# Kernel tuning notes

Hardware: AMD Instinct MI355X
Metric: run time of the kernel (lower is better)

## Reference

```python
import jax, jax.numpy as jnp
import numpy as np

N = 4096          # in_features
M = 4096          # out_features
RANK = 64
FT = 16           # ft_rank (trainable LoRA)
RES = RANK - FT   # frozen low-rank residual
CB = 65536        # E8P: 16-bit codeword per group of 8 weights
CW = 8            # codeword width (E8 lattice dim)
Q_SCALE = 0.02
GLOBAL_SCALE = 1.0


def _hadamard(n):
    # Sylvester construction, normalized: H @ H.T = I (matches matmul_hadU/hadUt up to transpose; H is symmetric)
    H = np.array([[1.0]], dtype=np.float32)
    while H.shape[0] < n:
        H = np.block([[H, H], [H, -H]])
    return H / np.sqrt(np.float32(n))


def setup_inputs() -> dict:
    key = jax.random.key(0)
    ks = jax.random.split(key, 9)
    x = jax.random.normal(ks[0], (8192, N), jnp.float32)
    Q_idxs = jax.random.randint(ks[1], (M, N // CW), 0, CB, dtype=jnp.int32)
    grid = jax.random.normal(ks[2], (CB, CW), jnp.float32) * 0.5   # E8P codebook grid
    SU = jax.random.rademacher(ks[3], (N,), dtype=jnp.float32)     # random sign vectors (QuIP#)
    SV = jax.random.rademacher(ks[4], (M,), dtype=jnp.float32)
    L_ft = jax.random.normal(ks[5], (M, FT), jnp.float32) * 0.02
    R_ft = jax.random.normal(ks[6], (FT, N), jnp.float32) * 0.02
    L_res = jax.random.normal(ks[7], (M, RES), jnp.float32) * 0.02
    R_res = jax.random.normal(ks[8], (RES, N), jnp.float32) * 0.02
    had_left = jnp.asarray(_hadamard(N))
    had_right = jnp.asarray(_hadamard(M))
    return {"x": x, "SU": SU, "SV": SV, "grid": grid, "L_ft": L_ft, "R_ft": R_ft,
            "L_res": L_res, "R_res": R_res, "had_left": had_left,
            "had_right": had_right, "Q_idxs": Q_idxs}


def reference(x, SU, SV, grid, L_ft, R_ft, L_res, R_res, had_left, had_right, Q_idxs):
    shape = x.shape
    h = x.reshape(-1, N) * SU                 # x * SU
    h = h @ had_left                          # matmul_hadUt (Hadamard is symmetric orthogonal)
    # E8P codebook decode: gather 8-dim codewords -> full [M, N] weight, fused matmul
    W = grid[Q_idxs].reshape(M, N)            # [M, N//8, 8] -> [M, N]
    out = (h @ W.T) * Q_SCALE                 # Q.forward
    out = out + (h @ R_res.T) @ L_res.T       # frozen low-rank residual (rank - ft_rank)
    out = out + (h @ R_ft.T) @ L_ft.T         # trainable LoRA path
    out = (out @ had_right) * GLOBAL_SCALE    # matmul_hadU * global_scale
    out = out * SV
    return out.reshape(*shape[:-1], M)
```

## Files before the change

kernel.cpp:

```cpp
#include <hip/hip_runtime.h>
#include <hip/hip_bf16.h>
#include <stdint.h>


typedef __bf16 bf16;
typedef __bf16 bf16x8 __attribute__((ext_vector_type(8)));
typedef float f32x4 __attribute__((ext_vector_type(4)));

#define KE 4160
#define KT_MAIN 130
#define NN 4096
#define MM 4096
#define BB 8192

__global__ void prep_kernel(const float* __restrict__ Lft, const float* __restrict__ Rft,
                            const float* __restrict__ Lres, const float* __restrict__ Rres,
                            bf16* __restrict__ Rcat, bf16* __restrict__ Wq) {
  int tid = blockIdx.x * 256 + threadIdx.x;
  if (tid < 64 * 4096) {
    int r = tid >> 12, n = tid & 4095;
    float v = (r < 48) ? Rres[r * 4096 + n] : Rft[(r - 48) * 4096 + n];
    Rcat[tid] = (bf16)v;
  } else {
    int t2 = tid - 64 * 4096;
    int m = t2 >> 6, r = t2 & 63;
    float v = (r < 48) ? Lres[m * 48 + r] : Lft[m * 16 + (r - 48)];
    Wq[(size_t)m * KE + 4096 + r] = (bf16)v;
  }
}

__global__ void decode_kernel(const int* __restrict__ qidx, const float* __restrict__ grid,
                              bf16* __restrict__ Wq) {
  int tid = blockIdx.x * 256 + threadIdx.x;
  int m = tid >> 9, g = tid & 511;
  uint32_t idx = (uint32_t)qidx[tid];
  const float4* gp = (const float4*)(grid + (size_t)idx * 8);
  float4 w0 = gp[0], w1 = gp[1];
  bf16x8 o;
  o[0] = (bf16)(w0.x * 0.02f); o[1] = (bf16)(w0.y * 0.02f);
  o[2] = (bf16)(w0.z * 0.02f); o[3] = (bf16)(w0.w * 0.02f);
  o[4] = (bf16)(w1.x * 0.02f); o[5] = (bf16)(w1.y * 0.02f);
  o[6] = (bf16)(w1.z * 0.02f); o[7] = (bf16)(w1.w * 0.02f);
  *(bf16x8*)(Wq + (size_t)m * KE + g * 8) = o;
}

__global__ void fwht_pre_kernel(const float* __restrict__ src,
                                bf16* __restrict__ dst,
                                const float* __restrict__ SU) {
  __shared__ float buf[4096];
  const int row = blockIdx.x, t = threadIdx.x;
  const float4* sp = (const float4*)(src + (size_t)row * NN + t * 16);
  const float4* su = (const float4*)(SU + t * 16);
  float v[16];
#pragma unroll
  for (int q = 0; q < 4; ++q) {
    float4 a = sp[q], s = su[q];
    v[q * 4 + 0] = a.x * s.x; v[q * 4 + 1] = a.y * s.y;
    v[q * 4 + 2] = a.z * s.z; v[q * 4 + 3] = a.w * s.w;
  }
#pragma unroll
  for (int s = 1; s < 16; s <<= 1) {
#pragma unroll
    for (int i = 0; i < 16; ++i) {
      if (!(i & s)) { float a = v[i], b = v[i + s]; v[i] = a + b; v[i + s] = a - b; }
    }
  }
#pragma unroll
  for (int i = 0; i < 16; ++i) buf[t * 16 + i] = v[i];
  for (int s = 16; s < 4096; s <<= 1) {
    __syncthreads();
#pragma unroll
    for (int j = 0; j < 8; ++j) {
      int p = t + j * 256;
      int i = ((p & ~(s - 1)) << 1) | (p & (s - 1));
      float a = buf[i], b = buf[i + s];
      buf[i] = a + b; buf[i + s] = a - b;
    }
  }
  __syncthreads();
  bf16x8 o0, o1;
#pragma unroll
  for (int i = 0; i < 8; ++i) {
    o0[i] = (bf16)(buf[t * 16 + i] * 0.015625f);
    o1[i] = (bf16)(buf[t * 16 + 8 + i] * 0.015625f);
  }
  bf16* dp = dst + (size_t)row * KE + t * 16;
  *(bf16x8*)dp = o0;
  *(bf16x8*)(dp + 8) = o1;
}

__global__ void fwht_post_kernel(float* __restrict__ data, const float* __restrict__ SV) {
  __shared__ float buf[4096];
  const int row = blockIdx.x, t = threadIdx.x;
  float4* dp = (float4*)(data + (size_t)row * MM + t * 16);
  float v[16];
#pragma unroll
  for (int q = 0; q < 4; ++q) {
    float4 a = dp[q];
    v[q * 4 + 0] = a.x; v[q * 4 + 1] = a.y; v[q * 4 + 2] = a.z; v[q * 4 + 3] = a.w;
  }
#pragma unroll
  for (int s = 1; s < 16; s <<= 1) {
#pragma unroll
    for (int i = 0; i < 16; ++i) {
      if (!(i & s)) { float a = v[i], b = v[i + s]; v[i] = a + b; v[i + s] = a - b; }
    }
  }
#pragma unroll
  for (int i = 0; i < 16; ++i) buf[t * 16 + i] = v[i];
  for (int s = 16; s < 4096; s <<= 1) {
    __syncthreads();
#pragma unroll
    for (int j = 0; j < 8; ++j) {
      int p = t + j * 256;
      int i = ((p & ~(s - 1)) << 1) | (p & (s - 1));
      float a = buf[i], b = buf[i + s];
      buf[i] = a + b; buf[i + s] = a - b;
    }
  }
  __syncthreads();
  const float4* sv = (const float4*)(SV + t * 16);
#pragma unroll
  for (int q = 0; q < 4; ++q) {
    float4 s = sv[q];
    float4 o;
    o.x = buf[t * 16 + q * 4 + 0] * 0.015625f * s.x;
    o.y = buf[t * 16 + q * 4 + 1] * 0.015625f * s.y;
    o.z = buf[t * 16 + q * 4 + 2] * 0.015625f * s.z;
    o.w = buf[t * 16 + q * 4 + 3] * 0.015625f * s.w;
    dp[q] = o;
  }
}

__global__ void __launch_bounds__(256) tgemm_kernel(const bf16* __restrict__ A,
                                                    const bf16* __restrict__ Bm,
                                                    float* __restrict__ Tpart) {
  __shared__ bf16 lA[128 * 32];
  __shared__ bf16 lB[64 * 32];
  const int t = threadIdx.x, w = t >> 6, l = t & 63;
  const int bmBlk = blockIdx.x;
  const int split = blockIdx.y;
  const int wm = w >> 1, wn = w & 1;
  f32x4 acc[4][2] = {};
  const int arow = t >> 1, acol = (t & 1) * 16;
  const bf16* pa = A + (size_t)(bmBlk * 128 + arow) * KE + acol;
  const int brow = (t & 127) >> 1, bcol = acol;
  const bf16* pb = Bm + (size_t)brow * 4096 + bcol;
  const int fr = l & 15, fk = (l >> 4) * 8;
  for (int kt = 0; kt < 32; ++kt) {
    const int k0 = (split * 32 + kt) * 32;
    bf16x8 a0 = *(const bf16x8*)(pa + k0);
    bf16x8 a1 = *(const bf16x8*)(pa + k0 + 8);
    *(bf16x8*)&lA[arow * 32 + acol] = a0;
    *(bf16x8*)&lA[arow * 32 + acol + 8] = a1;
    if (t < 128) {
      bf16x8 b0 = *(const bf16x8*)(pb + k0);
      bf16x8 b1 = *(const bf16x8*)(pb + k0 + 8);
      *(bf16x8*)&lB[brow * 32 + bcol] = b0;
      *(bf16x8*)&lB[brow * 32 + bcol + 8] = b1;
    }
    __syncthreads();
    bf16x8 af[4], bfr[2];
#pragma unroll
    for (int i = 0; i < 4; ++i) af[i] = *(const bf16x8*)&lA[(wm * 64 + i * 16 + fr) * 32 + fk];
#pragma unroll
    for (int i = 0; i < 2; ++i) bfr[i] = *(const bf16x8*)&lB[(wn * 32 + i * 16 + fr) * 32 + fk];
#pragma unroll
    for (int mi = 0; mi < 4; ++mi)
#pragma unroll
      for (int ni = 0; ni < 2; ++ni)
        acc[mi][ni] = __builtin_amdgcn_mfma_f32_16x16x32_bf16(af[mi], bfr[ni], acc[mi][ni], 0, 0, 0);
    __syncthreads();
  }
  float* out = Tpart + (size_t)split * BB * 64;
  const int orow = bmBlk * 128 + wm * 64 + (l >> 4) * 4;
  const int ocol = wn * 32 + (l & 15);
#pragma unroll
  for (int mi = 0; mi < 4; ++mi)
#pragma unroll
    for (int ni = 0; ni < 2; ++ni)
#pragma unroll
      for (int r = 0; r < 4; ++r)
        out[(size_t)(orow + mi * 16 + r) * 64 + ocol + ni * 16] = acc[mi][ni][r];
}

__global__ void tconv_kernel(const float* __restrict__ Tpart, bf16* __restrict__ h) {
  int i = blockIdx.x * 256 + threadIdx.x;
  float s = Tpart[i] + Tpart[i + BB * 64] + Tpart[i + 2 * BB * 64] + Tpart[i + 3 * BB * 64];
  int row = i >> 6, c = i & 63;
  h[(size_t)row * KE + 4096 + c] = (bf16)s;
}

__global__ void __launch_bounds__(256) mgemm_kernel(const bf16* __restrict__ A,
                                                    const bf16* __restrict__ B,
                                                    float* __restrict__ C) {
  __shared__ bf16 lA[128 * 32];
  __shared__ bf16 lB[128 * 32];
  const int t = threadIdx.x, w = t >> 6, l = t & 63;
  const int bn = blockIdx.x, bm = blockIdx.y;
  const int wm = w >> 1, wn = w & 1;
  f32x4 acc[4][4] = {};
  const int srow = t >> 1, scol = (t & 1) * 16;
  const bf16* pa = A + (size_t)(bm * 128 + srow) * KE + scol;
  const bf16* pb = B + (size_t)(bn * 128 + srow) * KE + scol;
  const int fr = l & 15, fk = (l >> 4) * 8;
  for (int kt = 0; kt < KT_MAIN; ++kt) {
    const int k0 = kt * 32;
    bf16x8 a0 = *(const bf16x8*)(pa + k0);
    bf16x8 a1 = *(const bf16x8*)(pa + k0 + 8);
    bf16x8 b0 = *(const bf16x8*)(pb + k0);
    bf16x8 b1 = *(const bf16x8*)(pb + k0 + 8);
    *(bf16x8*)&lA[srow * 32 + scol] = a0;
    *(bf16x8*)&lA[srow * 32 + scol + 8] = a1;
    *(bf16x8*)&lB[srow * 32 + scol] = b0;
    *(bf16x8*)&lB[srow * 32 + scol + 8] = b1;
    __syncthreads();
    bf16x8 af[4], bfr[4];
#pragma unroll
    for (int i = 0; i < 4; ++i) {
      af[i] = *(const bf16x8*)&lA[(wm * 64 + i * 16 + fr) * 32 + fk];
      bfr[i] = *(const bf16x8*)&lB[(wn * 64 + i * 16 + fr) * 32 + fk];
    }
#pragma unroll
    for (int mi = 0; mi < 4; ++mi)
#pragma unroll
      for (int ni = 0; ni < 4; ++ni)
        acc[mi][ni] = __builtin_amdgcn_mfma_f32_16x16x32_bf16(af[mi], bfr[ni], acc[mi][ni], 0, 0, 0);
    __syncthreads();
  }
  const int orow = bm * 128 + wm * 64 + (l >> 4) * 4;
  const int ocol = bn * 128 + wn * 64 + (l & 15);
#pragma unroll
  for (int mi = 0; mi < 4; ++mi)
#pragma unroll
    for (int ni = 0; ni < 4; ++ni)
#pragma unroll
      for (int r = 0; r < 4; ++r)
        C[(size_t)(orow + mi * 16 + r) * MM + ocol + ni * 16] = acc[mi][ni][r];
}

extern "C" void kernel_launch(void* const* d_in, const int* in_sizes, int n_in,
                              void* d_out, int out_size, void* d_ws, size_t ws_size,
                              hipStream_t stream) {
  const float* x    = (const float*)d_in[0];
  const float* SU   = (const float*)d_in[1];
  const float* SV   = (const float*)d_in[2];
  const float* grid = (const float*)d_in[3];
  const float* Lft  = (const float*)d_in[4];
  const float* Rft  = (const float*)d_in[5];
  const float* Lres = (const float*)d_in[6];
  const float* Rres = (const float*)d_in[7];
  const int*   qidx = (const int*)d_in[10];
  float* out = (float*)d_out;

  char* ws = (char*)d_ws;
  bf16*  h     = (bf16*)ws;
  bf16*  Wq    = (bf16*)(ws + 68157440);
  bf16*  Rcat  = (bf16*)(ws + 68157440 + 34078720);
  float* Tpart = (float*)(ws + 68157440 + 34078720 + 524288);

  prep_kernel<<<2048, 256, 0, stream>>>(Lft, Rft, Lres, Rres, Rcat, Wq);
  decode_kernel<<<8192, 256, 0, stream>>>(qidx, grid, Wq);
  fwht_pre_kernel<<<8192, 256, 0, stream>>>(x, h, SU);
  tgemm_kernel<<<dim3(64, 4), 256, 0, stream>>>(h, Rcat, Tpart);
  tconv_kernel<<<2048, 256, 0, stream>>>(Tpart, h);
  mgemm_kernel<<<dim3(32, 64), 256, 0, stream>>>(h, Wq, out);
  fwht_post_kernel<<<8192, 256, 0, stream>>>(out, SV);
}
```

Before: 753.2 us.

## Double-buffer LDS tiles in main GEMM with register prefetch of next k-tile

The main bf16 GEMM now keeps two LDS buffers per operand. The next k-tile is loaded from global memory into registers before the current tile's MFMAs run, and stored into the alternate buffer afterwards, with a single barrier per iteration. This is meant to hide global-load latency behind compute and remove one of the two barriers per k-step. It doubles shared memory use and adds some register pressure, which could reduce occupancy.

After: 760.1 us. Within noise of the previous version (+0.9%).

```diff
diff --git a/kernel.cpp b/kernel.cpp
--- a/kernel.cpp
+++ b/kernel.cpp
@@ -194,8 +194,8 @@
 __global__ void __launch_bounds__(256) mgemm_kernel(const bf16* __restrict__ A,
                                                     const bf16* __restrict__ B,
                                                     float* __restrict__ C) {
-  __shared__ bf16 lA[128 * 32];
-  __shared__ bf16 lB[128 * 32];
+  __shared__ bf16 lA[2][128 * 32];
+  __shared__ bf16 lB[2][128 * 32];
   const int t = threadIdx.x, w = t >> 6, l = t & 63;
   const int bn = blockIdx.x, bm = blockIdx.y;
   const int wm = w >> 1, wn = w & 1;
@@ -204,29 +204,46 @@
   const bf16* pa = A + (size_t)(bm * 128 + srow) * KE + scol;
   const bf16* pb = B + (size_t)(bn * 128 + srow) * KE + scol;
   const int fr = l & 15, fk = (l >> 4) * 8;
+  const int so = srow * 32 + scol;
+
+  bf16x8 a0 = *(const bf16x8*)(pa);
+  bf16x8 a1 = *(const bf16x8*)(pa + 8);
+  bf16x8 b0 = *(const bf16x8*)(pb);
+  bf16x8 b1 = *(const bf16x8*)(pb + 8);
+  *(bf16x8*)&lA[0][so] = a0;
+  *(bf16x8*)&lA[0][so + 8] = a1;
+  *(bf16x8*)&lB[0][so] = b0;
+  *(bf16x8*)&lB[0][so + 8] = b1;
+  __syncthreads();
+
   for (int kt = 0; kt < KT_MAIN; ++kt) {
-    const int k0 = kt * 32;
-    bf16x8 a0 = *(const bf16x8*)(pa + k0);
-    bf16x8 a1 = *(const bf16x8*)(pa + k0 + 8);
-    bf16x8 b0 = *(const bf16x8*)(pb + k0);
-    bf16x8 b1 = *(const bf16x8*)(pb + k0 + 8);
-    *(bf16x8*)&lA[srow * 32 + scol] = a0;
-    *(bf16x8*)&lA[srow * 32 + scol + 8] = a1;
-    *(bf16x8*)&lB[srow * 32 + scol] = b0;
-    *(bf16x8*)&lB[srow * 32 + scol + 8] = b1;
-    __syncthreads();
+    const int cur = kt & 1;
+    if (kt + 1 < KT_MAIN) {
+      const int k0 = (kt + 1) * 32;
+      a0 = *(const bf16x8*)(pa + k0);
+      a1 = *(const bf16x8*)(pa + k0 + 8);
+      b0 = *(const bf16x8*)(pb + k0);
+      b1 = *(const bf16x8*)(pb + k0 + 8);
+    }
     bf16x8 af[4], bfr[4];
 #pragma unroll
     for (int i = 0; i < 4; ++i) {
-      af[i] = *(const bf16x8*)&lA[(wm * 64 + i * 16 + fr) * 32 + fk];
-      bfr[i] = *(const bf16x8*)&lB[(wn * 64 + i * 16 + fr) * 32 + fk];
+      af[i] = *(const bf16x8*)&lA[cur][(wm * 64 + i * 16 + fr) * 32 + fk];
+      bfr[i] = *(const bf16x8*)&lB[cur][(wn * 64 + i * 16 + fr) * 32 + fk];
     }
 #pragma unroll
     for (int mi = 0; mi < 4; ++mi)
 #pragma unroll
       for (int ni = 0; ni < 4; ++ni)
         acc[mi][ni] = __builtin_amdgcn_mfma_f32_16x16x32_bf16(af[mi], bfr[ni], acc[mi][ni], 0, 0, 0);
-    __syncthreads();
+    if (kt + 1 < KT_MAIN) {
+      const int nxt = cur ^ 1;
+      *(bf16x8*)&lA[nxt][so] = a0;
+      *(bf16x8*)&lA[nxt][so + 8] = a1;
+      *(bf16x8*)&lB[nxt][so] = b0;
+      *(bf16x8*)&lB[nxt][so + 8] = b1;
+      __syncthreads();
+    }
   }
   const int orow = bm * 128 + wm * 64 + (l >> 4) * 4;
   const int ocol = bn * 128 + wn * 64 + (l & 15);
```
